# Optimization experiments

Hardware: AMD Instinct MI355X
Metric: run time of the kernel (lower is better)

The kernel has to match this reference:

```python
import jax, jax.numpy as jnp
import numpy as np

N_EMBEDS = 1024
N_HEADS = 16
HEAD_DIM = N_EMBEDS // N_HEADS
SCALE = HEAD_DIM ** (-0.5)
B, T = 2, 2048


def setup_inputs() -> dict:
    key = jax.random.key(0)
    k1, k2, k3, k4 = jax.random.split(key, 4)
    x = jax.random.normal(k1, (B, T, N_EMBEDS), dtype=jnp.float32)
    # Glorot-uniform-style init like keras Dense defaults (scale irrelevant for correctness)
    w_qkv = jax.random.normal(k2, (N_EMBEDS, 3 * N_EMBEDS), dtype=jnp.float32) * (N_EMBEDS ** -0.5)
    w_proj = jax.random.normal(k3, (N_EMBEDS, N_EMBEDS), dtype=jnp.float32) * (N_EMBEDS ** -0.5)
    b_proj = jnp.zeros((N_EMBEDS,), dtype=jnp.float32)
    return {"x": x, "w_qkv": w_qkv, "w_proj": w_proj, "b_proj": b_proj}


def reference(x, w_qkv, w_proj, b_proj):
    Bc, Tc, D = x.shape
    qkv = x @ w_qkv                                   # [B,T,3D]
    q, k, v = jnp.split(qkv, 3, axis=-1)
    def heads(t):
        return t.reshape(Bc, Tc, N_HEADS, HEAD_DIM).transpose(0, 2, 1, 3)  # [B,H,T,hd]
    q, k, v = heads(q), heads(k), heads(v)
    att = jnp.einsum("bhqd,bhkd->bhqk", q, k) * SCALE  # [B,H,T,T]
    causal = jnp.tril(jnp.ones((Tc, Tc), dtype=bool))[None, None]
    att = jnp.where(causal, att, jnp.float32(-1e9))
    att = jax.nn.softmax(att, axis=-1)
    out = jnp.einsum("bhqk,bhkd->bhqd", att, v)        # [B,H,T,hd]
    out = out.transpose(0, 2, 1, 3).reshape(Bc, Tc, D)
    return out @ w_proj + b_proj
```

## Files before the change

kernel.cpp:

```cpp
#include <hip/hip_runtime.h>
#include <hip/hip_bf16.h>


typedef __bf16 bf16;
typedef float f32x4 __attribute__((ext_vector_type(4)));
typedef float f32x16 __attribute__((ext_vector_type(16)));
typedef bf16 bf16x4 __attribute__((ext_vector_type(4)));
typedef bf16 bf16x8 __attribute__((ext_vector_type(8)));

#define B_ 2
#define T_ 2048
#define D_ 1024
#define H_ 16
#define HD_ 64
#define SEGS_PER_BH 15
#define PSLOTS 7

__device__ __forceinline__ f32x16 mfma32(bf16x8 a, bf16x8 b, f32x16 c) {
    return __builtin_amdgcn_mfma_f32_32x32x16_bf16(a, b, c, 0, 0, 0);
}

__device__ __forceinline__ void gload16(void* l, const void* g) {
    __builtin_amdgcn_global_load_lds(
        (const __attribute__((address_space(1))) unsigned int*)g,
        (__attribute__((address_space(3))) unsigned int*)l, 16, 0, 0);
}

__device__ __forceinline__ f32x16 z16() {
    f32x16 v;
#pragma unroll
    for (int i = 0; i < 16; ++i) v[i] = 0.f;
    return v;
}

__global__ __launch_bounds__(256) void prep(
    const float* __restrict__ x, bf16* __restrict__ xb,
    const float* __restrict__ wqkv, bf16* __restrict__ wqkvt) {
    __shared__ float tile[32][33];
    const int bid = blockIdx.x;
    const int tid = threadIdx.x;
    if (bid < 4096) {
        int i = bid * 256 + tid;
        float4 v = ((const float4*)x)[i];
        bf16x4 o = { (bf16)v.x, (bf16)v.y, (bf16)v.z, (bf16)v.w };
        ((bf16x4*)xb)[i] = o;
        return;
    }
    int r = bid - 4096;
    const int C = 3 * D_;
    int bx = r % 96, by = r / 96;
    const int tx = tid & 31, ty = tid >> 5;
    int cx = bx * 32 + tx;
    int r0 = by * 32;
#pragma unroll
    for (int j = 0; j < 32; j += 8)
        tile[ty + j][tx] = wqkv[(size_t)(r0 + ty + j) * C + cx];
    __syncthreads();
    int rx = r0 + tx;
    int c0 = bx * 32;
#pragma unroll
    for (int j = 0; j < 32; j += 8)
        wqkvt[(size_t)(c0 + ty + j) * D_ + rx] = (bf16)tile[tx][ty + j];
}

template <int MW, int NWN, int EPI>
__global__ __launch_bounds__(256) void gemm_k(
    const bf16* __restrict__ A, const bf16* __restrict__ Bt,
    int M, int N, int K,
    bf16* __restrict__ qb, bf16* __restrict__ kb, bf16* __restrict__ vt,
    const float* __restrict__ bias, float* __restrict__ outf) {
    constexpr int BM = 64 * MW;
    constexpr int BN = 64 * NWN;
    __shared__ bf16 sA[BM * 64];
    __shared__ bf16 sB[BN * 64];
    const int tid = threadIdx.x;
    const int wave = tid >> 6, lane = tid & 63;
    const int ln = lane & 31, hi = lane >> 5;
    const int wr = (wave >> 1) * (32 * MW);
    const int wc = (wave & 1) * (32 * NWN);
    const int m0 = blockIdx.x * BM, n0 = blockIdx.y * BN;

    f32x16 acc[MW][NWN];
#pragma unroll
    for (int mi = 0; mi < MW; ++mi)
#pragma unroll
        for (int ni = 0; ni < NWN; ++ni) acc[mi][ni] = z16();

    for (int k0 = 0; k0 < K; k0 += 64) {
        __syncthreads();
#pragma unroll
        for (int j = 0; j < 2 * MW; ++j) {
            int c = tid + 256 * j;
            int r = c >> 3, g = (c & 7) ^ (r & 7);
            gload16(&sA[c * 8], A + (size_t)(m0 + r) * K + k0 + 8 * g);
        }
#pragma unroll
        for (int j = 0; j < 2 * NWN; ++j) {
            int c = tid + 256 * j;
            int r = c >> 3, g = (c & 7) ^ (r & 7);
            gload16(&sB[c * 8], Bt + (size_t)(n0 + r) * K + k0 + 8 * g);
        }
        __syncthreads();
#pragma unroll
        for (int s = 0; s < 4; ++s) {
            bf16x8 av[MW], bv[NWN];
#pragma unroll
            for (int mi = 0; mi < MW; ++mi) {
                int r = wr + mi * 32 + ln;
                av[mi] = *(const bf16x8*)((const char*)sA + r * 128 +
                                          ((((s << 1) | hi) ^ (r & 7)) << 4));
            }
#pragma unroll
            for (int ni = 0; ni < NWN; ++ni) {
                int r = wc + ni * 32 + ln;
                bv[ni] = *(const bf16x8*)((const char*)sB + r * 128 +
                                          ((((s << 1) | hi) ^ (r & 7)) << 4));
            }
#pragma unroll
            for (int mi = 0; mi < MW; ++mi)
#pragma unroll
                for (int ni = 0; ni < NWN; ++ni)
                    acc[mi][ni] = mfma32(av[mi], bv[ni], acc[mi][ni]);
        }
    }

#pragma unroll
    for (int mi = 0; mi < MW; ++mi)
#pragma unroll
        for (int ni = 0; ni < NWN; ++ni) {
            int col = n0 + wc + ni * 32 + ln;
            if (EPI == 0) {
                int part = col >> 10, h = (col >> 6) & 15, d = col & 63;
                if (part == 2) {
#pragma unroll
                    for (int g4 = 0; g4 < 4; ++g4) {
                        int row = m0 + wr + mi * 32 + 8 * g4 + 4 * hi;
                        int bb = row >> 11, tt = row & (T_ - 1);
                        bf16x4 w;
#pragma unroll
                        for (int j = 0; j < 4; ++j)
                            w[j] = (bf16)acc[mi][ni][4 * g4 + j];
                        *(bf16x4*)&vt[(((size_t)(bb * H_ + h) * HD_) + d) * T_ + tt] = w;
                    }
                } else {
                    bf16* dst = (part == 0) ? qb : kb;
#pragma unroll
                    for (int r = 0; r < 16; ++r) {
                        int row = m0 + wr + mi * 32 + (r & 3) + 8 * (r >> 2) + 4 * hi;
                        int bb = row >> 11, tt = row & (T_ - 1);
                        dst[((size_t)(bb * H_ + h) * T_ + tt) * HD_ + d] =
                            (bf16)acc[mi][ni][r];
                    }
                }
            } else {
#pragma unroll
                for (int r = 0; r < 16; ++r) {
                    int row = m0 + wr + mi * 32 + (r & 3) + 8 * (r >> 2) + 4 * hi;
                    outf[(size_t)row * N + col] = acc[mi][ni][r] + bias[col];
                }
            }
        }
}

static __device__ const signed char QT_T[SEGS_PER_BH] =
    {5, 5, 2, 7, 7, 7, 6, 6, 4, 4, 6, 3, 3, 1, 0};
static __device__ const signed char SEG_T[SEGS_PER_BH] =
    {0, 1, -1, 0, 1, 2, 0, 1, 0, 1, 2, 0, 1, -1, -1};
static __device__ const signed char NS_T[SEGS_PER_BH] =
    {2, 2, 1, 3, 3, 3, 3, 3, 2, 2, 3, 2, 2, 1, 1};
static __device__ const signed char PSLOT_T[SEGS_PER_BH] =
    {0, 2, 0, 0, 5, 6, 0, 3, 0, 1, 4, 0, 0, 0, 0};

__device__ __forceinline__ bf16x8 kread(const char* base, int row, int s, int hi) {
    int b = (row * 128 + s * 32 + hi * 16) ^ ((row & 7) << 4);
    return *(const bf16x8*)(base + b);
}
__device__ __forceinline__ bf16x8 vread(const char* base, int row, int s, int hi) {
    int sw = (row & 7) << 4;
    int b0 = (row * 128 + s * 32 + hi * 8) ^ sw;
    int b1 = (row * 128 + s * 32 + hi * 8 + 16) ^ sw;
    bf16x4 lo = *(const bf16x4*)(base + b0);
    bf16x4 hi4 = *(const bf16x4*)(base + b1);
    return __builtin_shufflevector(lo, hi4, 0, 1, 2, 3, 4, 5, 6, 7);
}

__global__ __launch_bounds__(512, 4) void attn_kernel(
    const bf16* __restrict__ qb, const bf16* __restrict__ kb,
    const bf16* __restrict__ vtb, bf16* __restrict__ ob,
    bf16* __restrict__ oP, float2* __restrict__ mlP) {
    __shared__ bf16 sK2[2][4096];
    __shared__ bf16 sV2[2][4096];

    const int bid = blockIdx.x;
    const int bh = bid & 31;
    const int sid = bid >> 5;
    const int qt = QT_T[sid];
    const int seg = SEG_T[sid];
    const int ns = NS_T[sid];
    const int nt = 4 * qt + 4;
    int t0, t1;
    if (seg < 0) { t0 = 0; t1 = nt; }
    else {
        int len = (nt + ns - 1) / ns;
        t0 = seg * len;
        t1 = (t0 + len < nt) ? t0 + len : nt;
    }
    const int b = bh >> 4, h = bh & 15;
    const int tid = threadIdx.x, wave = tid >> 6, lane = tid & 63;
    const int ln = lane & 31, hi = lane >> 5;
    const int qs = qt * 256 + wave * 32;
    const int qrow = qs + ln;

    const bf16* Qg = qb + (size_t)bh * (T_ * HD_);
    const bf16* Kg = kb + (size_t)bh * (T_ * HD_);
    const bf16* Vtg = vtb + (size_t)bh * (HD_ * T_);

    bf16x8 qf[4];
#pragma unroll
    for (int s = 0; s < 4; ++s) {
        bf16x8 v = *(const bf16x8*)&Qg[(size_t)qrow * HD_ + s * 16 + hi * 8];
#pragma unroll
        for (int e = 0; e < 8; ++e) v[e] = (bf16)((float)v[e] * 0.1803368801f);
        qf[s] = v;
    }
    bf16x8 ones;
#pragma unroll
    for (int e = 0; e < 8; ++e) ones[e] = (bf16)1.0f;

    const int rr0 = tid >> 3;
    const int gg = ((tid & 7) ^ (rr0 & 7)) * 8;

    {
        int kv0 = t0 * 64;
        gload16(&sK2[0][tid * 8], Kg + (size_t)(kv0 + rr0) * HD_ + gg);
        gload16(&sV2[0][tid * 8], Vtg + (size_t)rr0 * T_ + kv0 + gg);
    }
    __syncthreads();

    const float NINF = -__builtin_inff();
    f32x16 oA = z16(), oB = z16();
    float mR = NINF, lR = 0.f;
    int cur = 0;

    for (int t = t0; t < t1; ++t) {
        if ((t + 1) < t1) {
            int kv0 = (t + 1) * 64;
            gload16(&sK2[cur ^ 1][tid * 8], Kg + (size_t)(kv0 + rr0) * HD_ + gg);
            gload16(&sV2[cur ^ 1][tid * 8], Vtg + (size_t)rr0 * T_ + kv0 + gg);
        }

        if (64 * t <= qs + 31) {
            const char* kbase = (const char*)sK2[cur];
            const char* vbase = (const char*)sV2[cur];

            f32x16 p0 = z16(), p1 = z16();
            __builtin_amdgcn_s_setprio(1);
#pragma unroll
            for (int s = 0; s < 4; ++s) {
                bf16x8 a0 = kread(kbase, ln, s, hi);
                bf16x8 a1 = kread(kbase, ln + 32, s, hi);
                p0 = mfma32(a0, qf[s], p0);
                p1 = mfma32(a1, qf[s], p1);
            }
            __builtin_amdgcn_s_setprio(0);

            if (64 * t + 63 > qs) {
                int kvb = 64 * t + 4 * hi;
#pragma unroll
                for (int r = 0; r < 16; ++r) {
                    int kvr = kvb + (r & 3) + 8 * (r >> 2);
                    if (kvr > qrow) p0[r] = NINF;
                    if (kvr + 32 > qrow) p1[r] = NINF;
                }
            }

            float mx0 = NINF, mx1 = NINF, mx2 = NINF, mx3 = NINF;
#pragma unroll
            for (int r = 0; r < 16; r += 4) {
                mx0 = fmaxf(fmaxf(p0[r], p1[r]), mx0);
                mx1 = fmaxf(fmaxf(p0[r + 1], p1[r + 1]), mx1);
                mx2 = fmaxf(fmaxf(p0[r + 2], p1[r + 2]), mx2);
                mx3 = fmaxf(fmaxf(p0[r + 3], p1[r + 3]), mx3);
            }
            float pm = fmaxf(fmaxf(mx0, mx1), fmaxf(mx2, mx3));
            pm = fmaxf(pm, __shfl_xor(pm, 32));

            if (__any(pm > mR + 8.f)) {
                float mnew = fmaxf(mR, pm);
                float fac = exp2f(mR - mnew);
                lR *= fac;
#pragma unroll
                for (int r = 0; r < 16; ++r) { oA[r] *= fac; oB[r] *= fac; }
                mR = mnew;
            }

            bf16x8 pa0, pa1, pa2, pa3;
#pragma unroll
            for (int e = 0; e < 8; ++e) {
                pa0[e] = (bf16)exp2f(p0[e] - mR);
                pa1[e] = (bf16)exp2f(p0[8 + e] - mR);
                pa2[e] = (bf16)exp2f(p1[e] - mR);
                pa3[e] = (bf16)exp2f(p1[8 + e] - mR);
            }

            __builtin_amdgcn_s_setprio(1);
            f32x16 sacc = mfma32(ones, pa0, z16());
            sacc = mfma32(ones, pa1, sacc);
            sacc = mfma32(ones, pa2, sacc);
            sacc = mfma32(ones, pa3, sacc);
#pragma unroll
            for (int s = 0; s < 4; ++s) {
                bf16x8 pas = (s == 0) ? pa0 : (s == 1) ? pa1 : (s == 2) ? pa2 : pa3;
                oA = mfma32(vread(vbase, ln, s, hi), pas, oA);
                oB = mfma32(vread(vbase, ln + 32, s, hi), pas, oB);
            }
            __builtin_amdgcn_s_setprio(0);
            lR += sacc[0];
        }

        __syncthreads();
        cur ^= 1;
    }

    if (seg < 0) {
        float inv = 1.f / lR;
        bf16* orow = ob + ((size_t)(b * T_ + qrow)) * D_ + h * HD_;
#pragma unroll
        for (int g = 0; g < 4; ++g) {
            bf16x4 w, w2;
#pragma unroll
            for (int j = 0; j < 4; ++j) {
                w[j] = (bf16)(oA[4 * g + j] * inv);
                w2[j] = (bf16)(oB[4 * g + j] * inv);
            }
            *(bf16x4*)&orow[4 * hi + 8 * g] = w;
            *(bf16x4*)&orow[32 + 4 * hi + 8 * g] = w2;
        }
    } else {
        int row = wave * 32 + ln;
        bf16* prow;
        if (seg == 0) {
            prow = ob + ((size_t)(b * T_ + qrow)) * D_ + h * HD_;
        } else {
            prow = oP + (((size_t)bh * PSLOTS + PSLOT_T[sid]) * 256 + row) * 64;
        }
#pragma unroll
        for (int g = 0; g < 4; ++g) {
            bf16x4 w, w2;
#pragma unroll
            for (int j = 0; j < 4; ++j) {
                w[j] = (bf16)oA[4 * g + j];
                w2[j] = (bf16)oB[4 * g + j];
            }
            *(bf16x4*)&prow[4 * hi + 8 * g] = w;
            *(bf16x4*)&prow[32 + 4 * hi + 8 * g] = w2;
        }
        if (hi == 0)
            mlP[(((size_t)bh * 5 + (qt - 3)) * 3 + seg) * 256 + row] =
                make_float2(mR, lR);
    }
}

__global__ __launch_bounds__(256) void attn_merge(
    const bf16* __restrict__ oP, const float2* __restrict__ mlP,
    bf16* __restrict__ ob,
    const float* __restrict__ wproj, bf16* __restrict__ wprojt) {
    __shared__ float tile[32][33];
    const int bid = blockIdx.x;
    const int tid = threadIdx.x;
    if (bid >= 160) {
        int r = bid - 160;
        int bx = r & 31, by = r >> 5;
        const int tx = tid & 31, ty = tid >> 5;
        int cx = bx * 32 + tx;
        int r0 = by * 32;
#pragma unroll
        for (int j = 0; j < 32; j += 8)
            tile[ty + j][tx] = wproj[(size_t)(r0 + ty + j) * D_ + cx];
        __syncthreads();
        int rx = r0 + tx;
        int c0 = bx * 32;
#pragma unroll
        for (int j = 0; j < 32; j += 8)
            wprojt[(size_t)(c0 + ty + j) * D_ + rx] = (bf16)tile[tx][ty + j];
        return;
    }
    int gid = bid * 256 + tid;
    int bh = gid / (5 * 256);
    int rem = gid - bh * (5 * 256);
    int strip = rem >> 8, row = rem & 255;
    int qt = strip + 3;
    int ns = (strip < 3) ? 2 : 3;
    int b = bh >> 4, h = bh & 15;
    int t = qt * 256 + row;
    int s1 = (strip < 3) ? strip : (strip == 3 ? 3 : 5);

    size_t mlb = ((size_t)bh * 5 + strip) * 3;
    float2 ml0 = mlP[(mlb + 0) * 256 + row];
    float2 ml1 = mlP[(mlb + 1) * 256 + row];
    float2 ml2 = (ns == 3) ? mlP[(mlb + 2) * 256 + row] : make_float2(-1e30f, 0.f);
    float ms = fmaxf(fmaxf(ml0.x, ml1.x), ml2.x);
    float w0 = exp2f(ml0.x - ms), w1 = exp2f(ml1.x - ms), w2 = exp2f(ml2.x - ms);
    if (ns < 3) w2 = 0.f;
    float inv = 1.f / (ml0.y * w0 + ml1.y * w1 + ml2.y * w2);
    w0 *= inv; w1 *= inv; w2 *= inv;

    bf16* dst = ob + ((size_t)(b * T_ + t)) * D_ + h * HD_;
    const bf16* r1 = oP + (((size_t)bh * PSLOTS + s1) * 256 + row) * 64;
    const bf16* r2 = oP + (((size_t)bh * PSLOTS + s1 + 1) * 256 + row) * 64;
#pragma unroll
    for (int g = 0; g < 8; ++g) {
        bf16x8 a = *(const bf16x8*)&dst[g * 8];
        bf16x8 c = *(const bf16x8*)&r1[g * 8];
        bf16x8 o;
        if (ns == 3) {
            bf16x8 d2 = *(const bf16x8*)&r2[g * 8];
#pragma unroll
            for (int j = 0; j < 8; ++j)
                o[j] = (bf16)((float)a[j] * w0 + (float)c[j] * w1 + (float)d2[j] * w2);
        } else {
#pragma unroll
            for (int j = 0; j < 8; ++j)
                o[j] = (bf16)((float)a[j] * w0 + (float)c[j] * w1);
        }
        *(bf16x8*)&dst[g * 8] = o;
    }
}

extern "C" void kernel_launch(void* const* d_in, const int* in_sizes, int n_in,
                              void* d_out, int out_size, void* d_ws, size_t ws_size,
                              hipStream_t stream) {
    const float* x = (const float*)d_in[0];
    const float* w_qkv = (const float*)d_in[1];
    const float* w_proj = (const float*)d_in[2];
    const float* b_proj = (const float*)d_in[3];
    float* out = (float*)d_out;
    char* ws = (char*)d_ws;

    bf16* xb = (bf16*)(ws);
    bf16* ob = (bf16*)(ws);
    bf16* wqkvt = (bf16*)(ws + 8388608);
    bf16* oP = (bf16*)(ws + 8388608);
    float2* mlP = (float2*)(ws + 15728640);
    bf16* qbuf = (bf16*)(ws + 16777216);
    bf16* kbuf = (bf16*)(ws + 25165824);
    bf16* wprojt = (bf16*)(ws + 25165824);
    bf16* vtbuf = (bf16*)(ws + 33554432);

    prep<<<7168, 256, 0, stream>>>(x, xb, w_qkv, wqkvt);

    gemm_k<2, 2, 0><<<dim3((B_ * T_) / 128, (3 * D_) / 128), 256, 0, stream>>>(
        xb, wqkvt, B_ * T_, 3 * D_, D_, qbuf, kbuf, vtbuf, nullptr, nullptr);

    attn_kernel<<<SEGS_PER_BH * 32, 512, 0, stream>>>(qbuf, kbuf, vtbuf, ob, oP, mlP);

    attn_merge<<<1184, 256, 0, stream>>>(oP, mlP, ob, w_proj, wprojt);

    gemm_k<1, 2, 1><<<dim3((B_ * T_) / 64, D_ / 128), 256, 0, stream>>>(
        ob, wprojt, B_ * T_, D_, D_, nullptr, nullptr, nullptr, b_proj, out);
}
```

Before: 117.2 us.

## Halve attention query tile to 128 rows with rebalanced split-KV schedule

```diff
diff --git a/kernel.cpp b/kernel.cpp
--- a/kernel.cpp
+++ b/kernel.cpp
@@ -13,8 +13,8 @@
 #define D_ 1024
 #define H_ 16
 #define HD_ 64
-#define SEGS_PER_BH 15
-#define PSLOTS 7
+#define SEGS_PER_BH 30
+#define PSLOTS 14
 
 __device__ __forceinline__ f32x16 mfma32(bf16x8 a, bf16x8 b, f32x16 c) {
     return __builtin_amdgcn_mfma_f32_32x32x16_bf16(a, b, c, 0, 0, 0);
@@ -163,13 +163,17 @@
 }
 
 static __device__ const signed char QT_T[SEGS_PER_BH] =
-    {5, 5, 2, 7, 7, 7, 6, 6, 4, 4, 6, 3, 3, 1, 0};
+    {12, 12, 11, 11, 10, 10, 15, 15, 4, 9, 9, 13, 13, 14, 14,
+     14, 15, 8, 8, 3, 7, 7, 13, 6, 6, 2, 5, 5, 1, 0};
 static __device__ const signed char SEG_T[SEGS_PER_BH] =
-    {0, 1, -1, 0, 1, 2, 0, 1, 0, 1, 2, 0, 1, -1, -1};
+    {0, 1, 0, 1, 0, 1, 0, 1, -1, 0, 1, 0, 1, 0, 1,
+     2, 2, 0, 1, -1, 0, 1, 2, 0, 1, -1, 0, 1, -1, -1};
 static __device__ const signed char NS_T[SEGS_PER_BH] =
-    {2, 2, 1, 3, 3, 3, 3, 3, 2, 2, 3, 2, 2, 1, 1};
+    {2, 2, 2, 2, 2, 2, 3, 3, 1, 2, 2, 3, 3, 3, 3,
+     3, 3, 2, 2, 1, 2, 2, 3, 2, 2, 1, 2, 2, 1, 1};
 static __device__ const signed char PSLOT_T[SEGS_PER_BH] =
-    {0, 2, 0, 0, 5, 6, 0, 3, 0, 1, 4, 0, 0, 0, 0};
+    {0, 7, 0, 6, 0, 5, 0, 12, 0, 0, 4, 0, 8, 0, 10,
+     11, 13, 0, 3, 0, 0, 2, 9, 0, 1, 0, 0, 0, 0, 0};
 
 __device__ __forceinline__ bf16x8 kread(const char* base, int row, int s, int hi) {
     int b = (row * 128 + s * 32 + hi * 16) ^ ((row & 7) << 4);
@@ -184,7 +188,7 @@
     return __builtin_shufflevector(lo, hi4, 0, 1, 2, 3, 4, 5, 6, 7);
 }
 
-__global__ __launch_bounds__(512, 4) void attn_kernel(
+__global__ __launch_bounds__(256, 3) void attn_kernel(
     const bf16* __restrict__ qb, const bf16* __restrict__ kb,
     const bf16* __restrict__ vtb, bf16* __restrict__ ob,
     bf16* __restrict__ oP, float2* __restrict__ mlP) {
@@ -197,7 +201,7 @@
     const int qt = QT_T[sid];
     const int seg = SEG_T[sid];
     const int ns = NS_T[sid];
-    const int nt = 4 * qt + 4;
+    const int nt = 2 * qt + 2;
     int t0, t1;
     if (seg < 0) { t0 = 0; t1 = nt; }
     else {
@@ -208,7 +212,7 @@
     const int b = bh >> 4, h = bh & 15;
     const int tid = threadIdx.x, wave = tid >> 6, lane = tid & 63;
     const int ln = lane & 31, hi = lane >> 5;
-    const int qs = qt * 256 + wave * 32;
+    const int qs = qt * 128 + wave * 32;
     const int qrow = qs + ln;
 
     const bf16* Qg = qb + (size_t)bh * (T_ * HD_);
@@ -233,7 +237,9 @@
     {
         int kv0 = t0 * 64;
         gload16(&sK2[0][tid * 8], Kg + (size_t)(kv0 + rr0) * HD_ + gg);
+        gload16(&sK2[0][(tid + 256) * 8], Kg + (size_t)(kv0 + rr0 + 32) * HD_ + gg);
         gload16(&sV2[0][tid * 8], Vtg + (size_t)rr0 * T_ + kv0 + gg);
+        gload16(&sV2[0][(tid + 256) * 8], Vtg + (size_t)(rr0 + 32) * T_ + kv0 + gg);
     }
     __syncthreads();
 
@@ -245,8 +251,12 @@
     for (int t = t0; t < t1; ++t) {
         if ((t + 1) < t1) {
             int kv0 = (t + 1) * 64;
-            gload16(&sK2[cur ^ 1][tid * 8], Kg + (size_t)(kv0 + rr0) * HD_ + gg);
-            gload16(&sV2[cur ^ 1][tid * 8], Vtg + (size_t)rr0 * T_ + kv0 + gg);
+            bf16* kd = sK2[cur ^ 1];
+            bf16* vd = sV2[cur ^ 1];
+            gload16(&kd[tid * 8], Kg + (size_t)(kv0 + rr0) * HD_ + gg);
+            gload16(&kd[(tid + 256) * 8], Kg + (size_t)(kv0 + rr0 + 32) * HD_ + gg);
+            gload16(&vd[tid * 8], Vtg + (size_t)rr0 * T_ + kv0 + gg);
+            gload16(&vd[(tid + 256) * 8], Vtg + (size_t)(rr0 + 32) * T_ + kv0 + gg);
         }
 
         if (64 * t <= qs + 31) {
@@ -342,7 +352,7 @@
         if (seg == 0) {
             prow = ob + ((size_t)(b * T_ + qrow)) * D_ + h * HD_;
         } else {
-            prow = oP + (((size_t)bh * PSLOTS + PSLOT_T[sid]) * 256 + row) * 64;
+            prow = oP + (((size_t)bh * PSLOTS + PSLOT_T[sid]) * 128 + row) * 64;
         }
 #pragma unroll
         for (int g = 0; g < 4; ++g) {
@@ -355,9 +365,11 @@
             *(bf16x4*)&prow[4 * hi + 8 * g] = w;
             *(bf16x4*)&prow[32 + 4 * hi + 8 * g] = w2;
         }
-        if (hi == 0)
-            mlP[(((size_t)bh * 5 + (qt - 3)) * 3 + seg) * 256 + row] =
-                make_float2(mR, lR);
+        if (hi == 0) {
+            int s = qt - 5;
+            int mlb = (s < 8) ? 2 * s : 16 + 3 * (s - 8);
+            mlP[((size_t)bh * 25 + mlb + seg) * 128 + row] = make_float2(mR, lR);
+        }
     }
 }
 
@@ -368,8 +380,8 @@
     __shared__ float tile[32][33];
     const int bid = blockIdx.x;
     const int tid = threadIdx.x;
-    if (bid >= 160) {
-        int r = bid - 160;
+    if (bid >= 176) {
+        int r = bid - 176;
         int bx = r & 31, by = r >> 5;
         const int tx = tid & 31, ty = tid >> 5;
         int cx = bx * 32 + tx;
@@ -386,19 +398,20 @@
         return;
     }
     int gid = bid * 256 + tid;
-    int bh = gid / (5 * 256);
-    int rem = gid - bh * (5 * 256);
-    int strip = rem >> 8, row = rem & 255;
-    int qt = strip + 3;
-    int ns = (strip < 3) ? 2 : 3;
+    int bh = gid / (11 * 128);
+    int rem = gid - bh * (11 * 128);
+    int strip = rem >> 7, row = rem & 127;
+    int qt = strip + 5;
+    int ns = (strip < 8) ? 2 : 3;
     int b = bh >> 4, h = bh & 15;
-    int t = qt * 256 + row;
-    int s1 = (strip < 3) ? strip : (strip == 3 ? 3 : 5);
-
-    size_t mlb = ((size_t)bh * 5 + strip) * 3;
-    float2 ml0 = mlP[(mlb + 0) * 256 + row];
-    float2 ml1 = mlP[(mlb + 1) * 256 + row];
-    float2 ml2 = (ns == 3) ? mlP[(mlb + 2) * 256 + row] : make_float2(-1e30f, 0.f);
+    int t = qt * 128 + row;
+    int mlb = (strip < 8) ? 2 * strip : 16 + 3 * (strip - 8);
+    int s1 = (strip < 8) ? strip : 8 + 2 * (strip - 8);
+
+    float2 ml0 = mlP[((size_t)bh * 25 + mlb + 0) * 128 + row];
+    float2 ml1 = mlP[((size_t)bh * 25 + mlb + 1) * 128 + row];
+    float2 ml2 = (ns == 3) ? mlP[((size_t)bh * 25 + mlb + 2) * 128 + row]
+                           : make_float2(-1e30f, 0.f);
     float ms = fmaxf(fmaxf(ml0.x, ml1.x), ml2.x);
     float w0 = exp2f(ml0.x - ms), w1 = exp2f(ml1.x - ms), w2 = exp2f(ml2.x - ms);
     if (ns < 3) w2 = 0.f;
@@ -406,8 +419,8 @@
     w0 *= inv; w1 *= inv; w2 *= inv;
 
     bf16* dst = ob + ((size_t)(b * T_ + t)) * D_ + h * HD_;
-    const bf16* r1 = oP + (((size_t)bh * PSLOTS + s1) * 256 + row) * 64;
-    const bf16* r2 = oP + (((size_t)bh * PSLOTS + s1 + 1) * 256 + row) * 64;
+    const bf16* r1 = oP + (((size_t)bh * PSLOTS + s1) * 128 + row) * 64;
+    const bf16* r2 = oP + (((size_t)bh * PSLOTS + s1 + 1) * 128 + row) * 64;
 #pragma unroll
     for (int g = 0; g < 8; ++g) {
         bf16x8 a = *(const bf16x8*)&dst[g * 8];
@@ -452,9 +465,9 @@
     gemm_k<2, 2, 0><<<dim3((B_ * T_) / 128, (3 * D_) / 128), 256, 0, stream>>>(
         xb, wqkvt, B_ * T_, 3 * D_, D_, qbuf, kbuf, vtbuf, nullptr, nullptr);
 
-    attn_kernel<<<SEGS_PER_BH * 32, 512, 0, stream>>>(qbuf, kbuf, vtbuf, ob, oP, mlP);
-
-    attn_merge<<<1184, 256, 0, stream>>>(oP, mlP, ob, w_proj, wprojt);
+    attn_kernel<<<SEGS_PER_BH * 32, 256, 0, stream>>>(qbuf, kbuf, vtbuf, ob, oP, mlP);
+
+    attn_merge<<<1200, 256, 0, stream>>>(oP, mlP, ob, w_proj, wprojt);
 
     gemm_k<1, 2, 1><<<dim3((B_ * T_) / 64, D_ / 128), 256, 0, stream>>>(
         ob, wprojt, B_ * T_, D_, D_, nullptr, nullptr, nullptr, b_proj, out);
```

After: 115.6 us. About the same (-1.3%).
